# Kernel optimization log

Hardware: AMD Instinct MI355X
Metric: run time of the kernel (lower is better)

Reference implementation:

```python
import jax, jax.numpy as jnp
import numpy as np

N_QUBITS = 8
N_LAYERS = 2


def _ry(theta):
    # theta: scalar or (B,) -> (...,2,2) complex64 RY matrix
    c = jnp.cos(theta * 0.5)
    s = jnp.sin(theta * 0.5)
    return jnp.stack([jnp.stack([c, -s], -1), jnp.stack([s, c], -1)], -2).astype(jnp.complex64)


def _rz(theta):
    # theta: scalar -> (2,2) complex64 RZ matrix diag(e^{-i t/2}, e^{i t/2})
    e = jnp.exp(-0.5j * theta.astype(jnp.complex64))
    z = jnp.zeros_like(e)
    return jnp.stack([jnp.stack([e, z], -1), jnp.stack([z, jnp.conj(e)], -1)], -2)


def _apply_1q(psi, U, wire):
    # U: (2,2) shared across batch; psi: (B, 2,2,...,2)
    ax = wire + 1
    psi = jnp.moveaxis(psi, ax, -1)
    psi = jnp.einsum('...i,ji->...j', psi, U)
    return jnp.moveaxis(psi, -1, ax)


def _apply_1q_batched(psi, U, wire):
    # U: (B,2,2) per-sample gate (angle embedding)
    ax = wire + 1
    psi = jnp.moveaxis(psi, ax, -1)
    psi = jnp.einsum('b...i,bji->b...j', psi, U)
    return jnp.moveaxis(psi, -1, ax)


def _apply_cnot(psi, ctrl, tgt):
    c_ax, t_ax = ctrl + 1, tgt + 1
    psi0 = jnp.take(psi, 0, axis=c_ax)
    psi1 = jnp.take(psi, 1, axis=c_ax)
    t2 = t_ax - 1 if t_ax > c_ax else t_ax
    psi1 = jnp.flip(psi1, axis=t2)  # X on target when control=1
    return jnp.stack([psi0, psi1], axis=c_ax)


def _circuit(x, weights):
    n = N_QUBITS
    B = x.shape[0]
    psi = jnp.zeros((B,) + (2,) * n, jnp.complex64)
    psi = psi.at[(slice(None),) + (0,) * n].set(1.0)
    ang = x * (np.pi / 2)
    for layer in range(weights.shape[0]):
        # AngleEmbedding: RY(x_i * pi/2) on each wire, per-sample angles
        for i in range(n):
            psi = _apply_1q_batched(psi, _ry(ang[:, i]), i)
        # trainable rotations
        for i in range(n):
            psi = _apply_1q(psi, _ry(weights[layer, i, 0]), i)
            psi = _apply_1q(psi, _rz(weights[layer, i, 1]), i)
        # CNOT ring
        for i in range(n - 1):
            psi = _apply_cnot(psi, i, i + 1)
        psi = _apply_cnot(psi, n - 1, 0)
    # <Z_i> = sum_s |psi_s|^2 * (+1 if bit_i(s)==0 else -1)
    p = (psi.real ** 2 + psi.imag ** 2).reshape(B, 2 ** n)
    bits = (jnp.arange(2 ** n)[:, None] >> (n - 1 - jnp.arange(n))) & 1
    zsign = (1 - 2 * bits).astype(jnp.float32)  # (256, 8)
    return (p @ zsign).astype(jnp.float32)


def setup_inputs() -> dict:
    key = jax.random.key(0)
    k1, k2 = jax.random.split(key)
    x = jax.random.uniform(k1, (65536, N_QUBITS), jnp.float32)
    weights = jax.random.uniform(k2, (N_LAYERS, N_QUBITS, 2), jnp.float32) * (2.0 * np.pi)
    return {"x": x, "weights": weights}


def reference(x, weights):
    return _circuit(x, weights)
```

## Files before the change

kernel.cpp:

```cpp
#include <hip/hip_runtime.h>

#define PI_OVER_2 1.57079632679489661923f


struct Bloch {
    float zB[8], xB[8], yB[8], C[8], S[8];
};

template <int QMIN, int QMAX>
__device__ __forceinline__ float dp_eval(const Bloch& B) {
    float re[16], im[16];
#pragma unroll
    for (int i = 0; i < 16; ++i) { re[i] = 0.f; im[i] = 0.f; }

    float zt = 1.f;
#pragma unroll
    for (int j = QMAX + 2; j < 8; ++j) zt *= B.zB[j];

#pragma unroll
    for (int gh = 0; gh < ((QMIN == 0) ? 2 : 1); ++gh) {
#pragma unroll
        for (int dl = 0; dl < 2; ++dl) {
            float v = dl ? -B.S[QMAX] : B.C[QMAX];
            if (gh) v *= zt;
            bool isY = false;
            if (QMAX < 7) {
                if (!dl && gh)      v *= B.zB[QMAX + 1];
                else if (dl && !gh) v *= B.xB[QMAX + 1];
                else if (dl && gh) { v *= B.yB[QMAX + 1]; isY = true; }
            }
            const int dt = (QMAX == 7) ? dl : 0;
            const int idx = dl | ((1 - dl) << 1) | (gh << 2) | (dt << 3);
            if (isY) im[idx] -= v; else re[idx] += v;
        }
    }

#pragma unroll
    for (int q = QMAX - 1; q >= QMIN; --q) {
        float nre[16], nim[16];
#pragma unroll
        for (int i = 0; i < 16; ++i) { nre[i] = 0.f; nim[i] = 0.f; }
#pragma unroll
        for (int st = 0; st < 16; ++st) {
            const int dp_ = st & 1, s1 = (st >> 1) & 1;
            const int g_ = (st >> 2) & 1, dt = (st >> 3) & 1;
            if (QMIN == 1 && g_) continue;
            if (QMAX < 7 && dt) continue;
#pragma unroll
            for (int dl = 0; dl < 2; ++dl) {
                const int mx = dl ^ dp_ ^ ((q == 0) ? dt : 0);
                const int mz = g_ ^ s1;
                float F = dl ? -B.S[q] : B.C[q];
                bool isY = false;
                if (!mx && mz)      F *= B.zB[q + 1];
                else if (mx && !mz) F *= B.xB[q + 1];
                else if (mx && mz) { F *= B.yB[q + 1]; isY = true; }
                const int ns = dl | ((s1 ^ 1 ^ dl) << 1) | (g_ << 2) | (dt << 3);
                if (isY) {
                    nre[ns] = fmaf(F, im[st], nre[ns]);
                    nim[ns] = fmaf(-F, re[st], nim[ns]);
                } else {
                    nre[ns] = fmaf(F, re[st], nre[ns]);
                    nim[ns] = fmaf(F, im[st], nim[ns]);
                }
            }
        }
#pragma unroll
        for (int i = 0; i < 16; ++i) { re[i] = nre[i]; im[i] = nim[i]; }
    }

    float acc = 0.f;
#pragma unroll
    for (int st = 0; st < 16; ++st) {
        const int dp_ = st & 1, sf = (st >> 1) & 1;
        const int g_ = (st >> 2) & 1, dt = (st >> 3) & 1;
        if (QMIN == 1 && g_) continue;
        if (QMAX < 7 && dt) continue;
        if (QMIN == 0 && g_ != (1 - dp_)) continue;
        float r = re[st], i = im[st];
#define APPLYG(MX, MZ, J)                                                     \
        if ((MX) == 0 && (MZ) == 1) { r *= B.zB[J]; i *= B.zB[J]; }           \
        else if ((MX) == 1 && (MZ) == 0) { r *= B.xB[J]; i *= B.xB[J]; }      \
        else if ((MX) == 1 && (MZ) == 1) {                                    \
            const float t = r; r = i * B.yB[J]; i = -t * B.yB[J]; }
        {
            const int mx0 = (QMIN == 0) ? (dp_ ^ dt) : dt;
            const int mz0 = (QMIN == 0) ? (sf ^ g_) : sf;
            APPLYG(mx0, mz0, 0)
        }
        if (QMIN == 1) {
            const int mx1 = dp_ ^ dt;
            const int mz1 = sf;
            APPLYG(mx1, mz1, 1)
        }
#undef APPLYG
        acc += r;
    }
    return acc;
}

__global__ __launch_bounds__(256) void qpauli_kernel(
        const float* __restrict__ x, const float* __restrict__ w,
        float* __restrict__ out, int nsamples) {
    const int gid = blockIdx.x * blockDim.x + threadIdx.x;
    const int wave = gid >> 6, lane = gid & 63;
    const int which = wave & 1;
    const int sample = (wave >> 1) * 64 + lane;
    if (sample >= nsamples) return;

    Bloch B;
    const float4* xv = reinterpret_cast<const float4*>(x + (size_t)sample * 8);
    const float4 xa = xv[0], xb = xv[1];
    const float xs[8] = {xa.x, xa.y, xa.z, xa.w, xb.x, xb.y, xb.z, xb.w};
#pragma unroll
    for (int q = 0; q < 8; ++q) {
        const float A1 = fmaf(xs[q], PI_OVER_2, w[2 * q]);
        const float W  = w[2 * q + 1];
        const float A2 = fmaf(xs[q], PI_OVER_2, w[16 + 2 * q]);
        float s1, c1, sw, cw;
        __sincosf(A1, &s1, &c1);
        __sincosf(W, &sw, &cw);
        __sincosf(A2, &B.S[q], &B.C[q]);
        B.zB[q] = c1;
        B.xB[q] = s1 * cw;
        B.yB[q] = s1 * sw;
    }

    float* o = out + (size_t)sample * 8;
    if (which == 0) {
        o[7] = dp_eval<0, 7>(B);
        o[1] = dp_eval<0, 1>(B);
        o[2] = dp_eval<0, 2>(B);
        o[4] = dp_eval<0, 4>(B);
    } else {
        o[0] = dp_eval<1, 7>(B);
        o[3] = dp_eval<0, 3>(B);
        o[5] = dp_eval<0, 5>(B);
        o[6] = dp_eval<0, 6>(B);
    }
}

extern "C" void kernel_launch(void* const* d_in, const int* in_sizes, int n_in,
                              void* d_out, int out_size, void* d_ws, size_t ws_size,
                              hipStream_t stream) {
    const float* x = (const float*)d_in[0];
    const float* w = (const float*)d_in[1];
    float* outp = (float*)d_out;
    const int nsamples = in_sizes[0] / 8;
    const int nthreads = nsamples * 2;
    const int block = 256;
    const int grid = (nthreads + block - 1) / block;
    qpauli_kernel<<<grid, block, 0, stream>>>(x, w, outp, nsamples);
}
```

Measured before the change: 9.876 us.

## Share forward and backward transfer-matrix sweeps across all eight qubit expectations

Replaces eight independent per-output transfer-matrix evaluations, split across two waves per sample, with one thread per sample. That thread runs a single forward sweep, which emits outputs 1 to 6 from running prefix states, and a single backward sweep, which yields outputs 0 and 7. This removes the repeated chain contractions that each output recomputed and halves the thread count. Each thread now does more serial work and holds more registers, which lowers parallelism. The output is written with two float4 stores.

```diff
diff --git a/kernel.cpp b/kernel.cpp
--- a/kernel.cpp
+++ b/kernel.cpp
@@ -3,141 +3,208 @@
 #define PI_OVER_2 1.57079632679489661923f
 
 
-struct Bloch {
-    float zB[8], xB[8], yB[8], C[8], S[8];
-};
-
-template <int QMIN, int QMAX>
-__device__ __forceinline__ float dp_eval(const Bloch& B) {
-    float re[16], im[16];
-#pragma unroll
-    for (int i = 0; i < 16; ++i) { re[i] = 0.f; im[i] = 0.f; }
-
-    float zt = 1.f;
-#pragma unroll
-    for (int j = QMAX + 2; j < 8; ++j) zt *= B.zB[j];
-
-#pragma unroll
-    for (int gh = 0; gh < ((QMIN == 0) ? 2 : 1); ++gh) {
-#pragma unroll
-        for (int dl = 0; dl < 2; ++dl) {
-            float v = dl ? -B.S[QMAX] : B.C[QMAX];
-            if (gh) v *= zt;
-            bool isY = false;
-            if (QMAX < 7) {
-                if (!dl && gh)      v *= B.zB[QMAX + 1];
-                else if (dl && !gh) v *= B.xB[QMAX + 1];
-                else if (dl && gh) { v *= B.yB[QMAX + 1]; isY = true; }
-            }
-            const int dt = (QMAX == 7) ? dl : 0;
-            const int idx = dl | ((1 - dl) << 1) | (gh << 2) | (dt << 3);
-            if (isY) im[idx] -= v; else re[idx] += v;
-        }
-    }
-
-#pragma unroll
-    for (int q = QMAX - 1; q >= QMIN; --q) {
-        float nre[16], nim[16];
-#pragma unroll
-        for (int i = 0; i < 16; ++i) { nre[i] = 0.f; nim[i] = 0.f; }
-#pragma unroll
-        for (int st = 0; st < 16; ++st) {
-            const int dp_ = st & 1, s1 = (st >> 1) & 1;
-            const int g_ = (st >> 2) & 1, dt = (st >> 3) & 1;
-            if (QMIN == 1 && g_) continue;
-            if (QMAX < 7 && dt) continue;
-#pragma unroll
-            for (int dl = 0; dl < 2; ++dl) {
-                const int mx = dl ^ dp_ ^ ((q == 0) ? dt : 0);
-                const int mz = g_ ^ s1;
-                float F = dl ? -B.S[q] : B.C[q];
-                bool isY = false;
-                if (!mx && mz)      F *= B.zB[q + 1];
-                else if (mx && !mz) F *= B.xB[q + 1];
-                else if (mx && mz) { F *= B.yB[q + 1]; isY = true; }
-                const int ns = dl | ((s1 ^ 1 ^ dl) << 1) | (g_ << 2) | (dt << 3);
-                if (isY) {
-                    nre[ns] = fmaf(F, im[st], nre[ns]);
-                    nim[ns] = fmaf(-F, re[st], nim[ns]);
-                } else {
-                    nre[ns] = fmaf(F, re[st], nre[ns]);
-                    nim[ns] = fmaf(F, im[st], nim[ns]);
-                }
-            }
-        }
-#pragma unroll
-        for (int i = 0; i < 16; ++i) { re[i] = nre[i]; im[i] = nim[i]; }
-    }
-
-    float acc = 0.f;
-#pragma unroll
-    for (int st = 0; st < 16; ++st) {
-        const int dp_ = st & 1, sf = (st >> 1) & 1;
-        const int g_ = (st >> 2) & 1, dt = (st >> 3) & 1;
-        if (QMIN == 1 && g_) continue;
-        if (QMAX < 7 && dt) continue;
-        if (QMIN == 0 && g_ != (1 - dp_)) continue;
-        float r = re[st], i = im[st];
-#define APPLYG(MX, MZ, J)                                                     \
-        if ((MX) == 0 && (MZ) == 1) { r *= B.zB[J]; i *= B.zB[J]; }           \
-        else if ((MX) == 1 && (MZ) == 0) { r *= B.xB[J]; i *= B.xB[J]; }      \
-        else if ((MX) == 1 && (MZ) == 1) {                                    \
-            const float t = r; r = i * B.yB[J]; i = -t * B.yB[J]; }
-        {
-            const int mx0 = (QMIN == 0) ? (dp_ ^ dt) : dt;
-            const int mz0 = (QMIN == 0) ? (sf ^ g_) : sf;
-            APPLYG(mx0, mz0, 0)
-        }
-        if (QMIN == 1) {
-            const int mx1 = dp_ ^ dt;
-            const int mz1 = sf;
-            APPLYG(mx1, mz1, 1)
-        }
-#undef APPLYG
-        acc += r;
-    }
-    return acc;
-}
-
-__global__ __launch_bounds__(256) void qpauli_kernel(
+__global__ __launch_bounds__(256) void qpauli2_kernel(
         const float* __restrict__ x, const float* __restrict__ w,
         float* __restrict__ out, int nsamples) {
-    const int gid = blockIdx.x * blockDim.x + threadIdx.x;
-    const int wave = gid >> 6, lane = gid & 63;
-    const int which = wave & 1;
-    const int sample = (wave >> 1) * 64 + lane;
+    const int sample = blockIdx.x * blockDim.x + threadIdx.x;
     if (sample >= nsamples) return;
 
-    Bloch B;
     const float4* xv = reinterpret_cast<const float4*>(x + (size_t)sample * 8);
     const float4 xa = xv[0], xb = xv[1];
     const float xs[8] = {xa.x, xa.y, xa.z, xa.w, xb.x, xb.y, xb.z, xb.w};
+
+    float C[8], S[8], zb[8], xbv[8], yb[8];
 #pragma unroll
     for (int q = 0; q < 8; ++q) {
         const float A1 = fmaf(xs[q], PI_OVER_2, w[2 * q]);
         const float W  = w[2 * q + 1];
         const float A2 = fmaf(xs[q], PI_OVER_2, w[16 + 2 * q]);
-        float s1, c1, sw, cw;
-        __sincosf(A1, &s1, &c1);
+        float s1v, c1v, sw, cw;
+        __sincosf(A1, &s1v, &c1v);
         __sincosf(W, &sw, &cw);
-        __sincosf(A2, &B.S[q], &B.C[q]);
-        B.zB[q] = c1;
-        B.xB[q] = s1 * cw;
-        B.yB[q] = s1 * sw;
-    }
-
-    float* o = out + (size_t)sample * 8;
-    if (which == 0) {
-        o[7] = dp_eval<0, 7>(B);
-        o[1] = dp_eval<0, 1>(B);
-        o[2] = dp_eval<0, 2>(B);
-        o[4] = dp_eval<0, 4>(B);
-    } else {
-        o[0] = dp_eval<1, 7>(B);
-        o[3] = dp_eval<0, 3>(B);
-        o[5] = dp_eval<0, 5>(B);
-        o[6] = dp_eval<0, 6>(B);
-    }
+        __sincosf(A2, &S[q], &C[q]);
+        zb[q] = c1v;
+        xbv[q] = s1v * cw;
+        yb[q] = s1v * sw;
+    }
+    float ZT[9];
+    ZT[8] = 1.f;
+#pragma unroll
+    for (int k = 7; k >= 2; --k) ZT[k] = zb[k] * ZT[k + 1];
+
+    float o[8];
+
+    float fre[16], fim[16];
+#pragma unroll
+    for (int i2 = 0; i2 < 16; ++i2) { fre[i2] = 0.f; fim[i2] = 0.f; }
+    fre[2] = C[0];
+    fre[6] = C[0] * zb[0];
+    fre[1] = -S[0] * xbv[0];
+    fim[5] = S[0] * yb[0];
+
+#define FSTEP(Q)                                                              \
+    {                                                                         \
+        const float Cz = C[Q] * zb[Q], Cx = C[Q] * xbv[Q], Cy = C[Q] * yb[Q]; \
+        const float Sz = S[Q] * zb[Q], Sx = S[Q] * xbv[Q], Sy = S[Q] * yb[Q]; \
+        float nre[16], nim[16];                                               \
+        _Pragma("unroll")                                                     \
+        for (int i2 = 0; i2 < 16; ++i2) { nre[i2] = 0.f; nim[i2] = 0.f; }     \
+        _Pragma("unroll")                                                     \
+        for (int st = 0; st < 16; ++st) {                                     \
+            const int dp_ = st & 1, z0 = (st >> 1) & 1;                       \
+            const int H = (st >> 2) & 1, P = (st >> 3) & 1;                   \
+            _Pragma("unroll")                                                 \
+            for (int d = 0; d < 2; ++d) {                                     \
+                const int mx = dp_ ^ d;                                       \
+                const int mz = z0 ^ H ^ P;                                    \
+                const int ns = d | (z0 << 1) | (H << 2) | ((P ^ d ^ 1) << 3); \
+                if (mx == 0 && mz == 0) {                                     \
+                    const float F = d ? -S[Q] : C[Q];                         \
+                    nre[ns] = fmaf(F, fre[st], nre[ns]);                      \
+                    nim[ns] = fmaf(F, fim[st], nim[ns]);                      \
+                } else if (mx == 0 && mz == 1) {                              \
+                    const float F = d ? -Sz : Cz;                             \
+                    nre[ns] = fmaf(F, fre[st], nre[ns]);                      \
+                    nim[ns] = fmaf(F, fim[st], nim[ns]);                      \
+                } else if (mx == 1 && mz == 0) {                              \
+                    const float F = d ? -Sx : Cx;                             \
+                    nre[ns] = fmaf(F, fre[st], nre[ns]);                      \
+                    nim[ns] = fmaf(F, fim[st], nim[ns]);                      \
+                } else {                \
+                    const float F = d ? -Sy : Cy;                             \
+                    nre[ns] = fmaf(F, fim[st], nre[ns]);                      \
+                    nim[ns] = fmaf(-F, fre[st], nim[ns]);                     \
+                }                                                             \
+            }                                                                 \
+        }                                                                     \
+        _Pragma("unroll")                                                     \
+        for (int i2 = 0; i2 < 16; ++i2) { fre[i2] = nre[i2]; fim[i2] = nim[i2]; } \
+    }
+
+#define FCLOSE(I)                                                             \
+    {                                                                         \
+        const float tz = ZT[(I) + 1];                    \
+        const float ty = yb[(I) + 1] * ZT[(I) + 2];                           \
+        const float tx = xbv[(I) + 1];                                        \
+        float acc = 0.f;                                                      \
+        _Pragma("unroll")                                                     \
+        for (int st = 0; st < 16; ++st) {                                     \
+            const int dp_ = st & 1, z0 = (st >> 1) & 1;                       \
+            const int H = (st >> 2) & 1, P = (st >> 3) & 1;                   \
+            if (H == P) {                                                     \
+                if (dp_ == 0 && z0 == 0)      acc += fre[st];                 \
+                else if (dp_ == 0 && z0 == 1) acc = fmaf(fre[st], tz, acc);   \
+                else if (dp_ == 1 && z0 == 0) acc = fmaf(fre[st], tx, acc);   \
+                else                          acc = fmaf(fim[st], ty, acc);   \
+            }                                                                 \
+        }                                                                     \
+        o[I] = acc;                                                           \
+    }
+
+    FSTEP(1) FCLOSE(1)
+    FSTEP(2) FCLOSE(2)
+    FSTEP(3) FCLOSE(3)
+    FSTEP(4) FCLOSE(4)
+    FSTEP(5) FCLOSE(5)
+    FSTEP(6) FCLOSE(6)
+#undef FSTEP
+#undef FCLOSE
+
+    float bre[16], bim[16];
+#pragma unroll
+    for (int i2 = 0; i2 < 16; ++i2) { bre[i2] = 0.f; bim[i2] = 0.f; }
+    bre[2] = C[7]; bre[6] = C[7];
+    bre[9] = -S[7]; bre[13] = -S[7];
+
+#define BSTEP(Q, ISQ0)                                                        \
+    {                                                                         \
+        const float Cz = C[Q] * zb[(Q) + 1], Cx = C[Q] * xbv[(Q) + 1];        \
+        const float Cy = C[Q] * yb[(Q) + 1];                                  \
+        const float Sz = S[Q] * zb[(Q) + 1], Sx = S[Q] * xbv[(Q) + 1];        \
+        const float Sy = S[Q] * yb[(Q) + 1];                                  \
+        float nre[16], nim[16];                                               \
+        _Pragma("unroll")                                                     \
+        for (int i2 = 0; i2 < 16; ++i2) { nre[i2] = 0.f; nim[i2] = 0.f; }     \
+        _Pragma("unroll")                                                     \
+        for (int st = 0; st < 16; ++st) {                                     \
+            const int dp_ = st & 1, s1 = (st >> 1) & 1;                       \
+            const int g = (st >> 2) & 1, dt = (st >> 3) & 1;                  \
+            _Pragma("unroll")                                                 \
+            for (int dl = 0; dl < 2; ++dl) {                                  \
+                const int mx = dl ^ dp_ ^ ((ISQ0) ? dt : 0);                  \
+                const int mz = g ^ s1;                                        \
+                const int ns = dl | ((s1 ^ 1 ^ dl) << 1) | (g << 2) | (dt << 3); \
+                if (mx == 0 && mz == 0) {                                     \
+                    const float F = dl ? -S[Q] : C[Q];                        \
+                    nre[ns] = fmaf(F, bre[st], nre[ns]);                      \
+                    nim[ns] = fmaf(F, bim[st], nim[ns]);                      \
+                } else if (mx == 0 && mz == 1) {                              \
+                    const float F = dl ? -Sz : Cz;                            \
+                    nre[ns] = fmaf(F, bre[st], nre[ns]);                      \
+                    nim[ns] = fmaf(F, bim[st], nim[ns]);                      \
+                } else if (mx == 1 && mz == 0) {                              \
+                    const float F = dl ? -Sx : Cx;                            \
+                    nre[ns] = fmaf(F, bre[st], nre[ns]);                      \
+                    nim[ns] = fmaf(F, bim[st], nim[ns]);                      \
+                } else {                                                      \
+                    const float F = dl ? -Sy : Cy;                            \
+                    nre[ns] = fmaf(F, bim[st], nre[ns]);                      \
+                    nim[ns] = fmaf(-F, bre[st], nim[ns]);                     \
+                }                                                             \
+            }                                                                 \
+        }                                                                     \
+        _Pragma("unroll")                                                     \
+        for (int i2 = 0; i2 < 16; ++i2) { bre[i2] = nre[i2]; bim[i2] = nim[i2]; } \
+    }
+
+    BSTEP(6, 0)
+    BSTEP(5, 0)
+    BSTEP(4, 0)
+    BSTEP(3, 0)
+    BSTEP(2, 0)
+    BSTEP(1, 0)
+
+#define APPLYG(MX, MZ, J)                                                     \
+    if ((MX) == 0 && (MZ) == 1) { r *= zb[J]; i *= zb[J]; }                   \
+    else if ((MX) == 1 && (MZ) == 0) { r *= xbv[J]; i *= xbv[J]; }            \
+    else if ((MX) == 1 && (MZ) == 1) {                                        \
+        const float t = r; r = i * yb[J]; i = -t * yb[J]; }
+
+    {
+        float acc = 0.f;
+#pragma unroll
+        for (int st = 0; st < 16; ++st) {
+            const int dp_ = st & 1, sf = (st >> 1) & 1;
+            const int g = (st >> 2) & 1, dt = (st >> 3) & 1;
+            if (g) continue;
+            float r = bre[st], i = bim[st];
+            APPLYG(dt, sf, 0)
+            APPLYG(dp_ ^ dt, sf, 1)
+            acc += r;
+        }
+        o[0] = acc;
+    }
+
+    BSTEP(0, 1)
+    {
+        float acc = 0.f;
+#pragma unroll
+        for (int st = 0; st < 16; ++st) {
+            const int dp_ = st & 1, sf = (st >> 1) & 1;
+            const int g = (st >> 2) & 1, dt = (st >> 3) & 1;
+            if (g != (1 ^ dp_)) continue;
+            float r = bre[st], i = bim[st];
+            APPLYG(dp_ ^ dt, sf ^ g, 0)
+            acc += r;
+        }
+        o[7] = acc;
+    }
+#undef APPLYG
+#undef BSTEP
+
+    float4* ov = reinterpret_cast<float4*>(out + (size_t)sample * 8);
+    ov[0] = make_float4(o[0], o[1], o[2], o[3]);
+    ov[1] = make_float4(o[4], o[5], o[6], o[7]);
 }
 
 extern "C" void kernel_launch(void* const* d_in, const int* in_sizes, int n_in,
@@ -147,8 +214,7 @@
     const float* w = (const float*)d_in[1];
     float* outp = (float*)d_out;
     const int nsamples = in_sizes[0] / 8;
-    const int nthreads = nsamples * 2;
     const int block = 256;
-    const int grid = (nthreads + block - 1) / block;
-    qpauli_kernel<<<grid, block, 0, stream>>>(x, w, outp, nsamples);
+    const int grid = (nsamples + block - 1) / block;
+    qpauli2_kernel<<<grid, block, 0, stream>>>(x, w, outp, nsamples);
 }
```

Measured after the change: 10.56 us. +6.9%, slower.
